# Optimization experiments

Hardware: AMD Instinct MI355X
Metric: run time of the kernel (lower is better)

## Reference

```python
import jax, jax.numpy as jnp
import numpy as np

S_MC = 4      # num_mc_samples
TEMP = 0.1    # soft_sampling temperature


def gcn_conv(x, adj, maskf, W, b):
    # DenseGCNConv: add self loops, sym-normalize, aggregate, linear, mask
    N = adj.shape[-1]
    A = adj + jnp.eye(N, dtype=adj.dtype)
    dis = jnp.clip(A.sum(-1), 1.0, None) ** -0.5
    A = dis[:, :, None] * A * dis[:, None, :]
    out = jnp.einsum('bij,bjf->bif', A, x @ W) + b
    return out * maskf[:, :, None]


def connected_components(adj, mask):
    # min-label propagation; labels in {1..N}, masked nodes -> 0
    B, N, _ = adj.shape
    labels0 = jnp.broadcast_to(jnp.arange(1, N + 1, dtype=jnp.int32), (B, N))
    big = jnp.int32(N + 2)
    adj_b = adj > 0
    def step(labels, _):
        nb = jnp.where(adj_b, labels[:, None, :], big)  # [B,N,N]
        return jnp.minimum(labels, nb.min(-1)), None
    labels, _ = jax.lax.scan(step, labels0, None, length=N)
    return jnp.where(mask, labels, 0)


def setup_inputs() -> dict:
    key = jax.random.key(0)
    ks = jax.random.split(key, 8)
    B, N, Fin, H, K = 512, 64, 128, 256, 32
    x = jax.random.normal(ks[0], (B, N, Fin), jnp.float32)
    lengths = jax.random.randint(ks[1], (B,), N // 2, N + 1)
    mask = jnp.arange(N)[None, :] < lengths[:, None]
    a = jax.random.uniform(ks[2], (B, N, N)) < 0.08
    adj = jnp.triu(a, 1)
    adj = (adj | jnp.swapaxes(adj, 1, 2)).astype(jnp.float32)
    adj = adj * mask[:, :, None] * mask[:, None, :]
    W1 = jax.random.normal(ks[3], (Fin, H), jnp.float32) / np.float32(np.sqrt(Fin))
    b1 = jnp.zeros((H,), jnp.float32)
    W2 = jax.random.normal(ks[4], (H, H), jnp.float32) / np.float32(np.sqrt(H))
    b2 = jnp.zeros((H,), jnp.float32)
    centroids = jax.random.normal(ks[5], (K, H), jnp.float32)
    return {'x': x, 'adj': adj, 'mask': mask, 'W1': W1, 'b1': b1, 'W2': W2, 'b2': b2, 'centroids': centroids}


def reference(x, adj, mask, W1, b1, W2, b2, centroids):
    B, N = mask.shape
    maskf = mask.astype(x.dtype)
    adj = adj * maskf[:, :, None] * maskf[:, None, :]
    # embedding convs
    h = jax.nn.relu(gcn_conv(x, adj, maskf, W1, b1))
    h = jax.nn.relu(gcn_conv(h, adj, maskf, W2, b2))
    # cdist to (detached) centroids, expanded form to avoid [B,N,K,F] blowup
    c = jax.lax.stop_gradient(centroids)
    d2 = (jnp.sum(h * h, -1, keepdims=True) + jnp.sum(c * c, -1)[None, None]
          - 2.0 * jnp.einsum('bnf,kf->bnk', h, c))
    dist = jnp.sqrt(jnp.clip(d2, 1e-12, None))  # [B,N,K]
    # softmin over clusters with temperature
    logits = -dist / TEMP
    probs = jax.nn.softmax(logits, -1)
    logp = jax.nn.log_softmax(logits, -1)
    # Categorical MC sampling via Gumbel-max
    g = jax.random.gumbel(jax.random.key(42), (S_MC,) + logp.shape, logp.dtype)
    concepts = jnp.argmax(logp[None] + g, -1).reshape(S_MC * B, N)  # [SB,N]
    # per-node sampled probability, product over valid nodes per graph (scatter mul)
    probs_r = jnp.tile(probs, (S_MC, 1, 1))
    node_p = jnp.take_along_axis(probs_r, concepts[..., None], -1)[..., 0]
    mask_r = jnp.tile(mask, (S_MC, 1))
    graph_prob = jnp.prod(jnp.where(mask_r, jax.lax.stop_gradient(node_p), 1.0), -1)  # [SB]
    # same-concept restricted adjacency -> connected components (undirected)
    adj_r = jnp.tile(adj, (S_MC, 1, 1))
    same = concepts[:, :, None] == concepts[:, None, :]
    adj_cc = jnp.where(same, adj_r, 0.0)
    adj_cc = jnp.maximum(adj_cc, jnp.swapaxes(adj_cc, 1, 2))
    labels = connected_components(adj_cc, mask_r)  # [SB,N], 0 reserved for masked
    # scatter-mean node embeddings per cluster; drop reserved cluster 0
    P = jax.nn.one_hot(labels, N + 1, dtype=x.dtype) * mask_r[..., None].astype(x.dtype)  # [SB,N,N+1]
    counts = P.sum(1)  # [SB,N+1]
    h_r = jnp.tile(h, (S_MC, 1, 1))
    new_x = (jnp.einsum('bnc,bnf->bcf', P, h_r) / jnp.clip(counts, 1.0, None)[..., None])[:, 1:, :]
    # pooled adjacency S^T A S, binarized
    new_adj = jnp.einsum('bic,bij,bjd->bcd', P, adj_r, P)[:, 1:, 1:]
    new_adj = (new_adj > 0).astype(x.dtype)
    return new_x, new_adj, graph_prob, labels
```

## Files before the change

kernel.cpp:

```cpp
#include <hip/hip_runtime.h>

#define B_    512
#define SB_   2048

static constexpr float TINYF = 1.17549435e-38f;
typedef float fx4  __attribute__((ext_vector_type(4)));
typedef short bf16x8 __attribute__((ext_vector_type(8)));
typedef float f32x4 __attribute__((ext_vector_type(4)));
typedef unsigned short u16x4 __attribute__((ext_vector_type(4)));

__device__ __forceinline__ unsigned tf_bits(unsigned lo) {
  const unsigned ks0 = 0u, ks1 = 42u, ks2 = 0x1BD11BF0u;
  unsigned x0 = 0u + ks0;
  unsigned x1 = lo + ks1;
#define TFR(r) { x0 += x1; x1 = (x1 << r) | (x1 >> (32 - r)); x1 ^= x0; }
  TFR(13) TFR(15) TFR(26) TFR(6)
  x0 += ks1; x1 += ks2 + 1u;
  TFR(17) TFR(29) TFR(16) TFR(24)
  x0 += ks2; x1 += ks0 + 2u;
  TFR(13) TFR(15) TFR(26) TFR(6)
  x0 += ks0; x1 += ks1 + 3u;
  TFR(17) TFR(29) TFR(16) TFR(24)
  x0 += ks1; x1 += ks2 + 4u;
  TFR(13) TFR(15) TFR(26) TFR(6)
  x0 += ks2; x1 += ks0 + 5u;
#undef TFR
  return x0 ^ x1;
}

__device__ __forceinline__ void split3(float v, unsigned& b1, unsigned& b2, unsigned& b3) {
  unsigned u1 = __float_as_uint(v) & 0xFFFF0000u;
  float r1 = v - __uint_as_float(u1);
  unsigned u2 = __float_as_uint(r1) & 0xFFFF0000u;
  float r2 = r1 - __uint_as_float(u2);
  unsigned u3 = __float_as_uint(r2) & 0xFFFF0000u;
  b1 = u1 >> 16; b2 = u2 >> 16; b3 = u3 >> 16;
}

__device__ __forceinline__ unsigned short planeOf(float v, int s) {
  unsigned u1 = __float_as_uint(v) & 0xFFFF0000u;
  if (s == 0) return (unsigned short)(u1 >> 16);
  float r1 = v - __uint_as_float(u1);
  unsigned u2 = __float_as_uint(r1) & 0xFFFF0000u;
  if (s == 1) return (unsigned short)(u2 >> 16);
  float r2 = r1 - __uint_as_float(u2);
  return (unsigned short)((__float_as_uint(r2) & 0xFFFF0000u) >> 16);
}

#define MF6(A0, A1, A2, Bv0, Bv1, Bv2, ACC)                                   \
  ACC = __builtin_amdgcn_mfma_f32_16x16x32_bf16(A0, Bv0, ACC, 0, 0, 0);       \
  ACC = __builtin_amdgcn_mfma_f32_16x16x32_bf16(A0, Bv1, ACC, 0, 0, 0);       \
  ACC = __builtin_amdgcn_mfma_f32_16x16x32_bf16(A1, Bv0, ACC, 0, 0, 0);       \
  ACC = __builtin_amdgcn_mfma_f32_16x16x32_bf16(A0, Bv2, ACC, 0, 0, 0);       \
  ACC = __builtin_amdgcn_mfma_f32_16x16x32_bf16(A1, Bv1, ACC, 0, 0, 0);       \
  ACC = __builtin_amdgcn_mfma_f32_16x16x32_bf16(A2, Bv0, ACC, 0, 0, 0);

__global__ __launch_bounds__(256) void k_init(const float* __restrict__ adj,
                                              const void* __restrict__ mptr,
                                              const float* __restrict__ W1,
                                              const float* __restrict__ W2,
                                              const float* __restrict__ cen,
                                              unsigned short* __restrict__ Ahat3,
                                              unsigned long long* __restrict__ nbr,
                                              float* __restrict__ maskf,
                                              unsigned short* __restrict__ Wg1,
                                              unsigned short* __restrict__ Wg2,
                                              unsigned short* __restrict__ cen3,
                                              float* __restrict__ ccbuf) {
  __shared__ float adjS[4096];
  __shared__ float AhS[64][65];
  __shared__ float dis[64];
  int b = blockIdx.x, tid = threadIdx.x;

  const float* ab = adj + (size_t)b * 4096;
  for (int i = tid; i < 4096; i += 256) adjS[i] = ab[i];
  __syncthreads();
  if (tid < 64) {
    float s = 0.0f;
    unsigned long long m = 0ull;
    for (int j = 0; j < 64; ++j) {
      float v = adjS[j * 64 + tid];
      s += (j == tid) ? (v + 1.0f) : v;
      if (v != 0.0f) m |= (1ull << j);
    }
    dis[tid] = 1.0f / sqrtf(fmaxf(s, 1.0f));
    nbr[b * 64 + tid] = m;
  }
  __syncthreads();
  for (int i = tid; i < 4096; i += 256) {
    int r = i >> 6, c = i & 63;
    float a = adjS[i] + ((r == c) ? 1.0f : 0.0f);
    AhS[r][c] = (dis[r] * a) * dis[c];
  }
  __syncthreads();
  unsigned short* dst = Ahat3 + (size_t)b * 12288;
  for (int ch = tid; ch < 1536; ch += 256) {
    int l15v = ch & 15, lgv = (ch >> 4) & 3, q2 = (ch >> 6) & 3, mt = (ch >> 8) & 1, s = ch >> 9;
    bf16x8 hv;
#pragma unroll
    for (int jj = 0; jj < 8; ++jj)
      hv[jj] = (short)planeOf(AhS[16 * q2 + l15v][32 * mt + 8 * lgv + jj], s);
    *(bf16x8*)&dst[(size_t)ch * 8] = hv;
  }

  if (b < 128) {
    __shared__ int s_ni, s_nf;
    if (tid == 0) { s_ni = 0; s_nf = 0; }
    __syncthreads();
    const unsigned* wp = (const unsigned*)mptr;
    int ni = 0, nf = 0;
    for (int i = tid; i < 2048; i += 256) {
      unsigned v = wp[i];
      if (v > 1u) ni = 1;
      if (v != 0u && v != 0x3f800000u) nf = 1;
    }
    if (ni) atomicOr(&s_ni, 1);
    if (nf) atomicOr(&s_nf, 1);
    __syncthreads();
    int fl = s_ni ? (s_nf ? 2 : 1) : 0;
    int i = b * 256 + tid;
    float r;
    if (fl == 0)      r = ((const int*)mptr)[i] ? 1.0f : 0.0f;
    else if (fl == 1) r = (((const float*)mptr)[i] != 0.0f) ? 1.0f : 0.0f;
    else              r = ((const unsigned char*)mptr)[i] ? 1.0f : 0.0f;
    maskf[i] = r;
  }

  int bi = b - 128;
  if (bi >= 0 && bi < 148) {
    if (bi < 144) {
      const float* W; unsigned short* Wg; int nk, s, ks, g;
      if (bi < 48) { W = W1; Wg = Wg1; nk = 4; s = bi >> 4; ks = (bi >> 2) & 3; g = bi & 3; }
      else { int t = bi - 48; W = W2; Wg = Wg2; nk = 8; s = t >> 5; ks = (t >> 2) & 7; g = t & 3; }
      int n = tid;
      bf16x8 hv;
#pragma unroll
      for (int jj = 0; jj < 8; ++jj) {
        float v = W[(size_t)(ks * 32 + g * 8 + jj) * 256 + n];
        hv[jj] = (short)planeOf(v, s);
      }
      *(bf16x8*)&Wg[((((size_t)s * nk + ks) * 4 + g) * 256 + n) * 8] = hv;
    } else if (bi == 144) {
      int k = tid >> 3, l8 = tid & 7;
      float s = 0.0f;
      for (int m = 0; m < 32; ++m) { float v = cen[k * 256 + l8 + 8 * m]; s += v * v; }
#pragma unroll
      for (int d = 1; d < 8; d <<= 1) s += __shfl_xor(s, d, 64);
      if (l8 == 0) ccbuf[k] = s;
    } else {
      int s = bi - 145;
      for (int u = 0; u < 4; ++u) {
        int idx = tid + 256 * u;
        int ks = idx >> 7, c = (idx >> 6) & 1, rem = idx & 63;
        int l15v = rem >> 2, lgv = rem & 3;
        bf16x8 hv;
#pragma unroll
        for (int jj = 0; jj < 8; ++jj)
          hv[jj] = (short)planeOf(cen[(size_t)(16 * c + l15v) * 256 + 32 * ks + 8 * lgv + jj], s);
        *(bf16x8*)&cen3[(size_t)s * 8192 + (size_t)idx * 8] = hv;
      }
    }
  }
}

__global__ __launch_bounds__(256, 2) void k_layer(const float* __restrict__ A,
                                                  const unsigned short* __restrict__ Wg,
                                                  const float* __restrict__ bias,
                                                  const unsigned short* __restrict__ Ahat3,
                                                  const float* __restrict__ maskf,
                                                  float* __restrict__ out, int nk) {
  __shared__ char smem[36864];
  __shared__ float biaS[256];
  __shared__ float maskS[64];
  unsigned short (*Ap)[3][2112] = (unsigned short(*)[3][2112])smem;
  unsigned short (*Tbuf)[72]    = (unsigned short(*)[72])smem;

  int b = blockIdx.x, tid = threadIdx.x;
  int w = tid >> 6, l = tid & 63;
  int l15 = l & 15, lg = l >> 4;
  int K = nk * 32;
  const float* Ab = A + (size_t)b * 64 * K;
  biaS[tid] = bias[tid];
  if (tid < 64) maskS[tid] = maskf[b * 64 + tid];

  int srow = tid >> 2, sg = tid & 3;
  const float* sp = Ab + (size_t)srow * K + sg * 8;

  {
    float4 v0 = *(const float4*)(sp);
    float4 v1 = *(const float4*)(sp + 4);
    float vv[8] = {v0.x, v0.y, v0.z, v0.w, v1.x, v1.y, v1.z, v1.w};
    bf16x8 p1, p2, p3;
#pragma unroll
    for (int jj = 0; jj < 8; ++jj) {
      unsigned h1, h2, h3; split3(vv[jj], h1, h2, h3);
      p1[jj] = (short)h1; p2[jj] = (short)h2; p3[jj] = (short)h3;
    }
    int off = sg * 528 + srow * 8;
    *(bf16x8*)&Ap[0][0][off] = p1;
    *(bf16x8*)&Ap[0][1][off] = p2;
    *(bf16x8*)&Ap[0][2][off] = p3;
  }
  __syncthreads();

  f32x4 acc1[4][4];
#pragma unroll
  for (int q = 0; q < 4; ++q)
#pragma unroll
    for (int c = 0; c < 4; ++c) acc1[q][c] = (f32x4){0.f, 0.f, 0.f, 0.f};

  const size_t wss = (size_t)nk * 8192;

  for (int ks = 0; ks < nk; ++ks) {
    int cur = ks & 1;
    float4 v0, v1;
    bool pf = (ks + 1 < nk);
    if (pf) {
      v0 = *(const float4*)(sp + (ks + 1) * 32);
      v1 = *(const float4*)(sp + (ks + 1) * 32 + 4);
    }
    bf16x8 af[4][3];
#pragma unroll
    for (int q = 0; q < 4; ++q) {
      int off = lg * 528 + (16 * q + l15) * 8;
#pragma unroll
      for (int s = 0; s < 3; ++s) af[q][s] = *(const bf16x8*)&Ap[cur][s][off];
    }
#pragma unroll
    for (int c = 0; c < 4; ++c) {
      size_t wbase = (((size_t)ks * 4 + lg) * 256 + (64 * w + 16 * c + l15)) * 8;
      bf16x8 b0 = *(const bf16x8*)&Wg[wbase];
      bf16x8 b1 = *(const bf16x8*)&Wg[wbase + wss];
      bf16x8 b2 = *(const bf16x8*)&Wg[wbase + 2 * wss];
#pragma unroll
      for (int q = 0; q < 4; ++q) {
        MF6(af[q][0], af[q][1], af[q][2], b0, b1, b2, acc1[q][c]);
      }
    }
    if (pf) {
      float vv[8] = {v0.x, v0.y, v0.z, v0.w, v1.x, v1.y, v1.z, v1.w};
      bf16x8 p1, p2, p3;
#pragma unroll
      for (int jj = 0; jj < 8; ++jj) {
        unsigned h1, h2, h3; split3(vv[jj], h1, h2, h3);
        p1[jj] = (short)h1; p2[jj] = (short)h2; p3[jj] = (short)h3;
      }
      int off = sg * 528 + srow * 8;
      *(bf16x8*)&Ap[cur ^ 1][0][off] = p1;
      *(bf16x8*)&Ap[cur ^ 1][1][off] = p2;
      *(bf16x8*)&Ap[cur ^ 1][2][off] = p3;
    }
    __syncthreads();
  }

  f32x4 acc2[4][4];
#pragma unroll
  for (int q = 0; q < 4; ++q)
#pragma unroll
    for (int c = 0; c < 4; ++c) acc2[q][c] = (f32x4){0.f, 0.f, 0.f, 0.f};

  const unsigned short* Ah = Ahat3 + (size_t)b * 12288;
#pragma unroll
  for (int sB = 0; sB < 3; ++sB) {
    const int nA = 3 - sB;
    __syncthreads();
#pragma unroll
    for (int q = 0; q < 4; ++q)
#pragma unroll
      for (int c = 0; c < 4; ++c) {
        u16x4 pv;
#pragma unroll
        for (int r = 0; r < 4; ++r) pv[r] = planeOf(acc1[q][c][r], sB);
        *(u16x4*)&Tbuf[64 * w + 16 * c + l15][16 * q + 4 * lg] = pv;
      }
    __syncthreads();
#pragma unroll
    for (int mt = 0; mt < 2; ++mt) {
      bf16x8 bf[4];
#pragma unroll
      for (int c = 0; c < 4; ++c)
        bf[c] = *(const bf16x8*)&Tbuf[64 * w + 16 * c + l15][32 * mt + 8 * lg];
#pragma unroll
      for (int q2 = 0; q2 < 4; ++q2) {
        bf16x8 afr[3];
#pragma unroll
        for (int sA = 0; sA < 3; ++sA)
          if (sA < nA)
            afr[sA] = *(const bf16x8*)&Ah[((((size_t)(sA * 2 + mt) * 4 + q2) * 4 + lg) * 16 + l15) * 8];
#pragma unroll
        for (int c = 0; c < 4; ++c)
#pragma unroll
          for (int sA = 0; sA < 3; ++sA)
            if (sA < nA)
              acc2[q2][c] = __builtin_amdgcn_mfma_f32_16x16x32_bf16(afr[sA], bf[c], acc2[q2][c], 0, 0, 0);
      }
    }
  }

#pragma unroll
  for (int q2 = 0; q2 < 4; ++q2) {
#pragma unroll
    for (int c = 0; c < 4; ++c) {
      int n = 64 * w + 16 * c + l15;
      float bv = biaS[n];
#pragma unroll
      for (int r = 0; r < 4; ++r) {
        int row = 16 * q2 + 4 * lg + r;
        float val = (acc2[q2][c][r] + bv) * maskS[row];
        out[((size_t)b * 64 + row) * 256 + n] = fmaxf(val, 0.0f);
      }
    }
  }
}

__global__ __launch_bounds__(256) void k_cdist(const float* __restrict__ h,
                                               const unsigned short* __restrict__ cen3,
                                               const float* __restrict__ ccbuf,
                                               int* __restrict__ conc,
                                               float* __restrict__ pp) {
  __shared__ float hS[16384];
  __shared__ float Dred[4][64][36];
  __shared__ float hhp[64][4];
  __shared__ float lgp[64][33];
  __shared__ float mxs[64], lgden[64];

  int b = blockIdx.x, tid = threadIdx.x;
  int w = tid >> 6, l = tid & 63, l15 = l & 15, lg = l >> 4;
  const float* hb = h + (size_t)b * 16384;

#pragma unroll
  for (int i = 0; i < 16; ++i) {
    int g = tid + 256 * i;
    float4 v = *(const float4*)&hb[(size_t)g * 4];
    int row = g >> 6;
    int fb = ((g & 63) * 16) ^ ((row & 7) << 4);
    *(float4*)((char*)&hS[row * 256] + fb) = v;
  }
  __syncthreads();

#define LD4(row, fbyte) (*(const float4*)((const char*)&hS[(row) * 256] + ((fbyte) ^ (((row) & 7) << 4))))

  {
    int row = tid & 63, qt = tid >> 6;
    float s = 0.0f;
    for (int u = 0; u < 16; ++u) {
      float4 v = LD4(row, qt * 256 + u * 16);
      s += v.x * v.x + v.y * v.y + v.z * v.z + v.w * v.w;
    }
    hhp[row][qt] = s;
  }

  f32x4 acc[4][2];
#pragma unroll
  for (int qt = 0; qt < 4; ++qt)
#pragma unroll
    for (int c = 0; c < 2; ++c) acc[qt][c] = (f32x4){0.f, 0.f, 0.f, 0.f};

#pragma unroll
  for (int ks2 = 0; ks2 < 2; ++ks2) {
    int ks = 2 * w + ks2;
#pragma unroll
    for (int qt = 0; qt < 4; ++qt) {
      int row = 16 * qt + l15;
      int fb = (32 * ks + 8 * lg) * 4;
      float4 v0 = LD4(row, fb);
      float4 v1 = LD4(row, fb + 16);
      float vv[8] = {v0.x, v0.y, v0.z, v0.w, v1.x, v1.y, v1.z, v1.w};
      bf16x8 a0, a1, a2;
#pragma unroll
      for (int jj = 0; jj < 8; ++jj) {
        unsigned h1, h2, h3; split3(vv[jj], h1, h2, h3);
        a0[jj] = (short)h1; a1[jj] = (short)h2; a2[jj] = (short)h3;
      }
#pragma unroll
      for (int c = 0; c < 2; ++c) {
        const unsigned short* cb = cen3 + ((size_t)(ks * 2 + c) * 64 + l15 * 4 + lg) * 8;
        bf16x8 b0 = *(const bf16x8*)cb;
        bf16x8 b1 = *(const bf16x8*)(cb + 8192);
        bf16x8 b2 = *(const bf16x8*)(cb + 16384);
        MF6(a0, a1, a2, b0, b1, b2, acc[qt][c]);
      }
    }
  }

#pragma unroll
  for (int qt = 0; qt < 4; ++qt)
#pragma unroll
    for (int c = 0; c < 2; ++c)
#pragma unroll
      for (int r = 0; r < 4; ++r)
        Dred[w][16 * qt + 4 * lg + r][16 * c + l15] = acc[qt][c][r];
  __syncthreads();

  {
    int n = tid >> 2, kq = tid & 3;
    float hh = (hhp[n][0] + hhp[n][1]) + (hhp[n][2] + hhp[n][3]);
#pragma unroll
    for (int j = 0; j < 8; ++j) {
      int k = kq * 8 + j;
      float dot = (Dred[0][n][k] + Dred[1][n][k]) + (Dred[2][n][k] + Dred[3][n][k]);
      float d2 = (hh + ccbuf[k]) - 2.0f * dot;
      lgp[n][k] = -10.0f * sqrtf(fmaxf(d2, 1e-12f));
    }
  }
  __syncthreads();

  if (tid < 64) {
    float mx = -1e30f;
    for (int k = 0; k < 32; ++k) mx = fmaxf(mx, lgp[tid][k]);
    float den = 0.0f;
    for (int k = 0; k < 32; ++k) den += expf(lgp[tid][k] - mx);
    mxs[tid] = mx; lgden[tid] = logf(den);
  }
  __syncthreads();
  for (int p = tid; p < 2048; p += 256) {
    int n = p >> 5, k = p & 31;
    lgp[n][k] = (lgp[n][k] - mxs[n]) - lgden[n];
  }
  __syncthreads();

  int hw = tid >> 5, k = tid & 31;
  for (int pass = 0; pass < 8; ++pass) {
    int n = hw * 8 + pass;
    float lp = lgp[n][k];
#pragma unroll
    for (int s4 = 0; s4 < 4; ++s4) {
      unsigned flat = (unsigned)(s4 * 32768 + b * 64 + n) * 32u + (unsigned)k;
      unsigned bits = tf_bits(flat);
      float fu = __uint_as_float((bits >> 9) | 0x3f800000u) - 1.0f;
      float u = fmaxf(TINYF, fu * (1.0f - TINYF) + TINYF);
      float g = -logf(-logf(u));
      float v = lp + g;
      int bi = k;
#pragma unroll
      for (int d = 1; d < 32; d <<= 1) {
        float ov = __shfl_xor(v, d, 32);
        int oi = __shfl_xor(bi, d, 32);
        if (ov > v || (ov == v && oi < bi)) { v = ov; bi = oi; }
      }
      if (k == 0) {
        conc[s4 * 32768 + b * 64 + n] = bi;
        pp[s4 * 32768 + b * 64 + n] = expf(lgp[n][bi]);
      }
    }
  }
#undef LD4
}

__global__ __launch_bounds__(256) void k_postx(const int* __restrict__ conc,
                                               const float* __restrict__ pp,
                                               const float* __restrict__ maskf,
                                               const unsigned long long* __restrict__ nbr,
                                               const float* __restrict__ h,
                                               float* __restrict__ out_gp,
                                               float* __restrict__ out_lab,
                                               float* __restrict__ out_newadj,
                                               float* __restrict__ out_newx) {
  int sb = blockIdx.x, b = sb & 511, tid = threadIdx.x;
  __shared__ int cs[64];
  __shared__ int lab[64];
  __shared__ unsigned long long sm_[64];
  __shared__ unsigned long long nbs[64];
  __shared__ unsigned long long clmaskS[64];
  __shared__ float o[4096];
  __shared__ int chg;

  for (int i = tid; i < 4096; i += 256) o[i] = 0.0f;
  bool mk = false;
  if (tid < 64) {
    cs[tid] = conc[sb * 64 + tid];
    nbs[tid] = nbr[b * 64 + tid];
    mk = maskf[b * 64 + tid] != 0.0f;
    lab[tid] = tid + 1;
  }
  if (tid == 0) chg = 0;
  __syncthreads();
  if (tid < 64) {
    unsigned long long nb = nbs[tid], s = 0ull;
    int c = cs[tid];
    while (nb) { int j = __ffsll(nb) - 1; if (cs[j] == c) s |= (1ull << j); nb &= nb - 1; }
    sm_[tid] = s;
  }
  __syncthreads();
  for (int it = 0; it < 64; ++it) {
    int m = 0;
    if (tid < 64) {
      m = lab[tid];
      unsigned long long t = sm_[tid];
      while (t) { int j = __ffsll(t) - 1; m = min(m, lab[j]); t &= t - 1; }
    }
    __syncthreads();
    if (tid < 64 && m < lab[tid]) { lab[tid] = m; chg = 1; }
    __syncthreads();
    if (chg == 0) break;
    __syncthreads();
    if (tid == 0) chg = 0;
  }
  if (tid < 64) {
    int lf = mk ? lab[tid] : 0;
    cs[tid] = lf;
    out_lab[sb * 64 + tid] = (float)lf;
    float pv = mk ? pp[sb * 64 + tid] : 1.0f;
#pragma unroll
    for (int d = 1; d < 64; d <<= 1) pv *= __shfl_xor(pv, d, 64);
    if (tid == 0) out_gp[sb] = pv;
  }
  __syncthreads();
  if (tid < 64) {
    unsigned long long cm = 0ull;
    for (int j = 0; j < 64; ++j)
      if (cs[j] == tid + 1) cm |= (1ull << j);
    clmaskS[tid] = cm;
  }
  for (int p = tid; p < 4096; p += 256) {
    int i = p >> 6, j = p & 63;
    int li = cs[i], lj = cs[j];
    if (li > 0 && lj > 0 && ((nbs[i] >> j) & 1ull))
      o[(li - 1) * 64 + (lj - 1)] = 1.0f;
  }
  __syncthreads();
  float* dst = out_newadj + (size_t)sb * 4096;
  for (int i = tid; i < 1024; i += 256) {
    fx4 v = ((const fx4*)o)[i];
    __builtin_nontemporal_store(v, (fx4*)dst + i);
  }

  int q = tid & 63, cp = tid >> 6;
  const float* hb = h + (size_t)b * 16384;
  for (int step = 0; step < 16; ++step) {
    int c = cp * 16 + step;
    unsigned long long m = clmaskS[c];
    float4 acc = make_float4(0.f, 0.f, 0.f, 0.f);
    unsigned long long t = m;
    while (t) {
      int j = __ffsll(t) - 1; t &= t - 1;
      float4 v = *(const float4*)&hb[j * 256 + q * 4];
      acc.x += v.x; acc.y += v.y; acc.z += v.z; acc.w += v.w;
    }
    int cnt = __popcll(m);
    float cf = (float)(cnt > 0 ? cnt : 1);
    fx4 r;
    r.x = acc.x / cf; r.y = acc.y / cf; r.z = acc.z / cf; r.w = acc.w / cf;
    __builtin_nontemporal_store(r, (fx4*)&out_newx[((size_t)sb * 64 + c) * 256 + q * 4]);
  }
}

extern "C" void kernel_launch(void* const* d_in, const int* in_sizes, int n_in,
                              void* d_out, int out_size, void* d_ws, size_t ws_size,
                              hipStream_t stream) {
  (void)in_sizes; (void)n_in; (void)out_size; (void)ws_size;
  const float* x   = (const float*)d_in[0];
  const float* adj = (const float*)d_in[1];
  const void*  mp  = d_in[2];
  const float* W1  = (const float*)d_in[3];
  const float* b1  = (const float*)d_in[4];
  const float* W2  = (const float*)d_in[5];
  const float* b2  = (const float*)d_in[6];
  const float* cen = (const float*)d_in[7];

  char* ws = (char*)d_ws;
  unsigned short* Ahat3 = (unsigned short*)(ws + 0);
  unsigned short* Wg1   = (unsigned short*)(ws + 12582912);
  unsigned short* Wg2   = (unsigned short*)(ws + 12779520);
  unsigned short* cen3  = (unsigned short*)(ws + 13172736);
  float* ccbuf          = (float*)(ws + 13221888);
  unsigned long long* nbr = (unsigned long long*)(ws + 13222016);
  float* maskf          = (float*)(ws + 13484160);
  int*   conc           = (int*)(ws + 13615232);
  float* pp             = (float*)(ws + 14139520);
  float* bufB           = (float*)(ws + 16777216);

  float* out        = (float*)d_out;
  float* out_newx   = out;
  float* out_newadj = out + 33554432;
  float* out_gp     = out + 41943040;
  float* out_lab    = out + 41945088;
  float* bufA       = out;

  hipLaunchKernelGGL(k_init,  dim3(512), dim3(256), 0, stream, adj, mp, W1, W2, cen,
                     Ahat3, nbr, maskf, Wg1, Wg2, cen3, ccbuf);
  hipLaunchKernelGGL(k_layer, dim3(512), dim3(256), 0, stream, x,    Wg1, b1, Ahat3, maskf, bufA, 4);
  hipLaunchKernelGGL(k_layer, dim3(512), dim3(256), 0, stream, bufA, Wg2, b2, Ahat3, maskf, bufB, 8);
  hipLaunchKernelGGL(k_cdist, dim3(512), dim3(256), 0, stream, bufB, cen3, ccbuf, conc, pp);
  hipLaunchKernelGGL(k_postx, dim3(2048), dim3(256), 0, stream, conc, pp, maskf, nbr, bufB,
                     out_gp, out_lab, out_newadj, out_newx);
}
```

Baseline: 180.6 us.

## Fuse per-graph pipeline into one mega-kernel with LDS-resident activations

Merges adjacency normalization, both GCN layers, cdist/sampling and cluster pooling into a single per-graph kernel. Intermediate hidden states, the normalized adjacency planes, neighbor masks and concepts stay in shared memory instead of round-tripping through global memory. Each of the 4 MC samples is handled by one wavefront, with wave-level early exit in label propagation. This removes several launches and global traffic, but uses large LDS (one block per CU) and only 512 blocks, which lowers occupancy and parallelism for the post-processing stage.

New measurement: 180.1 us. No clear change (-0.2%).

```diff
diff --git a/kernel.cpp b/kernel.cpp
--- a/kernel.cpp
+++ b/kernel.cpp
@@ -1,7 +1,6 @@
 #include <hip/hip_runtime.h>
 
 #define B_    512
-#define SB_   2048
 
 static constexpr float TINYF = 1.17549435e-38f;
 typedef float fx4  __attribute__((ext_vector_type(4)));
@@ -55,141 +54,74 @@
   ACC = __builtin_amdgcn_mfma_f32_16x16x32_bf16(A1, Bv1, ACC, 0, 0, 0);       \
   ACC = __builtin_amdgcn_mfma_f32_16x16x32_bf16(A2, Bv0, ACC, 0, 0, 0);
 
-__global__ __launch_bounds__(256) void k_init(const float* __restrict__ adj,
-                                              const void* __restrict__ mptr,
-                                              const float* __restrict__ W1,
-                                              const float* __restrict__ W2,
-                                              const float* __restrict__ cen,
-                                              unsigned short* __restrict__ Ahat3,
-                                              unsigned long long* __restrict__ nbr,
-                                              float* __restrict__ maskf,
-                                              unsigned short* __restrict__ Wg1,
-                                              unsigned short* __restrict__ Wg2,
-                                              unsigned short* __restrict__ cen3,
-                                              float* __restrict__ ccbuf) {
-  __shared__ float adjS[4096];
-  __shared__ float AhS[64][65];
-  __shared__ float dis[64];
-  int b = blockIdx.x, tid = threadIdx.x;
-
-  const float* ab = adj + (size_t)b * 4096;
-  for (int i = tid; i < 4096; i += 256) adjS[i] = ab[i];
-  __syncthreads();
-  if (tid < 64) {
+__global__ void k_setup(const float* __restrict__ W1, const float* __restrict__ W2,
+                        const float* __restrict__ cen,
+                        unsigned short* __restrict__ Wg1, unsigned short* __restrict__ Wg2,
+                        unsigned short* __restrict__ cen3, float* __restrict__ ccbuf) {
+  int bi = blockIdx.x, tid = threadIdx.x;
+  if (bi < 144) {
+    const float* W; unsigned short* Wg; int nk, s, ks, g;
+    if (bi < 48) { W = W1; Wg = Wg1; nk = 4; s = bi >> 4; ks = (bi >> 2) & 3; g = bi & 3; }
+    else { int t = bi - 48; W = W2; Wg = Wg2; nk = 8; s = t >> 5; ks = (t >> 2) & 7; g = t & 3; }
+    int n = tid;
+    bf16x8 hv;
+#pragma unroll
+    for (int jj = 0; jj < 8; ++jj) {
+      float v = W[(size_t)(ks * 32 + g * 8 + jj) * 256 + n];
+      hv[jj] = (short)planeOf(v, s);
+    }
+    *(bf16x8*)&Wg[((((size_t)s * nk + ks) * 4 + g) * 256 + n) * 8] = hv;
+  } else if (bi == 144) {
+    int k = tid >> 3, l8 = tid & 7;
     float s = 0.0f;
-    unsigned long long m = 0ull;
-    for (int j = 0; j < 64; ++j) {
-      float v = adjS[j * 64 + tid];
-      s += (j == tid) ? (v + 1.0f) : v;
-      if (v != 0.0f) m |= (1ull << j);
-    }
-    dis[tid] = 1.0f / sqrtf(fmaxf(s, 1.0f));
-    nbr[b * 64 + tid] = m;
-  }
-  __syncthreads();
-  for (int i = tid; i < 4096; i += 256) {
-    int r = i >> 6, c = i & 63;
-    float a = adjS[i] + ((r == c) ? 1.0f : 0.0f);
-    AhS[r][c] = (dis[r] * a) * dis[c];
-  }
-  __syncthreads();
-  unsigned short* dst = Ahat3 + (size_t)b * 12288;
-  for (int ch = tid; ch < 1536; ch += 256) {
-    int l15v = ch & 15, lgv = (ch >> 4) & 3, q2 = (ch >> 6) & 3, mt = (ch >> 8) & 1, s = ch >> 9;
-    bf16x8 hv;
-#pragma unroll
-    for (int jj = 0; jj < 8; ++jj)
-      hv[jj] = (short)planeOf(AhS[16 * q2 + l15v][32 * mt + 8 * lgv + jj], s);
-    *(bf16x8*)&dst[(size_t)ch * 8] = hv;
-  }
-
-  if (b < 128) {
-    __shared__ int s_ni, s_nf;
-    if (tid == 0) { s_ni = 0; s_nf = 0; }
-    __syncthreads();
-    const unsigned* wp = (const unsigned*)mptr;
-    int ni = 0, nf = 0;
-    for (int i = tid; i < 2048; i += 256) {
-      unsigned v = wp[i];
-      if (v > 1u) ni = 1;
-      if (v != 0u && v != 0x3f800000u) nf = 1;
-    }
-    if (ni) atomicOr(&s_ni, 1);
-    if (nf) atomicOr(&s_nf, 1);
-    __syncthreads();
-    int fl = s_ni ? (s_nf ? 2 : 1) : 0;
-    int i = b * 256 + tid;
-    float r;
-    if (fl == 0)      r = ((const int*)mptr)[i] ? 1.0f : 0.0f;
-    else if (fl == 1) r = (((const float*)mptr)[i] != 0.0f) ? 1.0f : 0.0f;
-    else              r = ((const unsigned char*)mptr)[i] ? 1.0f : 0.0f;
-    maskf[i] = r;
-  }
-
-  int bi = b - 128;
-  if (bi >= 0 && bi < 148) {
-    if (bi < 144) {
-      const float* W; unsigned short* Wg; int nk, s, ks, g;
-      if (bi < 48) { W = W1; Wg = Wg1; nk = 4; s = bi >> 4; ks = (bi >> 2) & 3; g = bi & 3; }
-      else { int t = bi - 48; W = W2; Wg = Wg2; nk = 8; s = t >> 5; ks = (t >> 2) & 7; g = t & 3; }
-      int n = tid;
+    for (int m = 0; m < 32; ++m) { float v = cen[k * 256 + l8 + 8 * m]; s += v * v; }
+#pragma unroll
+    for (int d = 1; d < 8; d <<= 1) s += __shfl_xor(s, d, 64);
+    if (l8 == 0) ccbuf[k] = s;
+  } else {
+    int s = bi - 145;
+    for (int u = 0; u < 4; ++u) {
+      int idx = tid + 256 * u;
+      int ks = idx >> 7, c = (idx >> 6) & 1, rem = idx & 63;
+      int l15v = rem >> 2, lgv = rem & 3;
       bf16x8 hv;
 #pragma unroll
-      for (int jj = 0; jj < 8; ++jj) {
-        float v = W[(size_t)(ks * 32 + g * 8 + jj) * 256 + n];
-        hv[jj] = (short)planeOf(v, s);
-      }
-      *(bf16x8*)&Wg[((((size_t)s * nk + ks) * 4 + g) * 256 + n) * 8] = hv;
-    } else if (bi == 144) {
-      int k = tid >> 3, l8 = tid & 7;
-      float s = 0.0f;
-      for (int m = 0; m < 32; ++m) { float v = cen[k * 256 + l8 + 8 * m]; s += v * v; }
-#pragma unroll
-      for (int d = 1; d < 8; d <<= 1) s += __shfl_xor(s, d, 64);
-      if (l8 == 0) ccbuf[k] = s;
-    } else {
-      int s = bi - 145;
-      for (int u = 0; u < 4; ++u) {
-        int idx = tid + 256 * u;
-        int ks = idx >> 7, c = (idx >> 6) & 1, rem = idx & 63;
-        int l15v = rem >> 2, lgv = rem & 3;
-        bf16x8 hv;
-#pragma unroll
-        for (int jj = 0; jj < 8; ++jj)
-          hv[jj] = (short)planeOf(cen[(size_t)(16 * c + l15v) * 256 + 32 * ks + 8 * lgv + jj], s);
-        *(bf16x8*)&cen3[(size_t)s * 8192 + (size_t)idx * 8] = hv;
-      }
-    }
-  }
-}
-
-__global__ __launch_bounds__(256, 2) void k_layer(const float* __restrict__ A,
-                                                  const unsigned short* __restrict__ Wg,
-                                                  const float* __restrict__ bias,
-                                                  const unsigned short* __restrict__ Ahat3,
-                                                  const float* __restrict__ maskf,
-                                                  float* __restrict__ out, int nk) {
-  __shared__ char smem[36864];
-  __shared__ float biaS[256];
-  __shared__ float maskS[64];
-  unsigned short (*Ap)[3][2112] = (unsigned short(*)[3][2112])smem;
-  unsigned short (*Tbuf)[72]    = (unsigned short(*)[72])smem;
-
-  int b = blockIdx.x, tid = threadIdx.x;
+      for (int jj = 0; jj < 8; ++jj)
+        hv[jj] = (short)planeOf(cen[(size_t)(16 * c + l15v) * 256 + 32 * ks + 8 * lgv + jj], s);
+      *(bf16x8*)&cen3[(size_t)s * 8192 + (size_t)idx * 8] = hv;
+    }
+  }
+}
+
+template<bool SRCL>
+__device__ __forceinline__ void layer_core(const float* __restrict__ Aglob,
+                                           const float (*hsrc)[260],
+                                           float (*hdst)[260],
+                                           const unsigned short* __restrict__ Wg, int nk,
+                                           const unsigned short* AhP,
+                                           const float* biaS, const float* maskS,
+                                           char* U, int tid) {
+  unsigned short (*Ap)[3][2112] = (unsigned short(*)[3][2112])U;
+  unsigned short (*Tbuf)[72]    = (unsigned short(*)[72])U;
   int w = tid >> 6, l = tid & 63;
   int l15 = l & 15, lg = l >> 4;
   int K = nk * 32;
-  const float* Ab = A + (size_t)b * 64 * K;
-  biaS[tid] = bias[tid];
-  if (tid < 64) maskS[tid] = maskf[b * 64 + tid];
-
   int srow = tid >> 2, sg = tid & 3;
-  const float* sp = Ab + (size_t)srow * K + sg * 8;
+  const float* sp = SRCL ? (const float*)nullptr : (Aglob + (size_t)srow * K + sg * 8);
 
   {
-    float4 v0 = *(const float4*)(sp);
-    float4 v1 = *(const float4*)(sp + 4);
-    float vv[8] = {v0.x, v0.y, v0.z, v0.w, v1.x, v1.y, v1.z, v1.w};
+    float vv[8];
+    if (SRCL) {
+      float4 v0 = *(const float4*)&hsrc[srow][sg * 8];
+      float4 v1 = *(const float4*)&hsrc[srow][sg * 8 + 4];
+      vv[0] = v0.x; vv[1] = v0.y; vv[2] = v0.z; vv[3] = v0.w;
+      vv[4] = v1.x; vv[5] = v1.y; vv[6] = v1.z; vv[7] = v1.w;
+    } else {
+      float4 v0 = *(const float4*)(sp);
+      float4 v1 = *(const float4*)(sp + 4);
+      vv[0] = v0.x; vv[1] = v0.y; vv[2] = v0.z; vv[3] = v0.w;
+      vv[4] = v1.x; vv[5] = v1.y; vv[6] = v1.z; vv[7] = v1.w;
+    }
     bf16x8 p1, p2, p3;
 #pragma unroll
     for (int jj = 0; jj < 8; ++jj) {
@@ -213,11 +145,20 @@
 
   for (int ks = 0; ks < nk; ++ks) {
     int cur = ks & 1;
-    float4 v0, v1;
+    float vv[8];
     bool pf = (ks + 1 < nk);
     if (pf) {
-      v0 = *(const float4*)(sp + (ks + 1) * 32);
-      v1 = *(const float4*)(sp + (ks + 1) * 32 + 4);
+      if (SRCL) {
+        float4 v0 = *(const float4*)&hsrc[srow][(ks + 1) * 32 + sg * 8];
+        float4 v1 = *(const float4*)&hsrc[srow][(ks + 1) * 32 + sg * 8 + 4];
+        vv[0] = v0.x; vv[1] = v0.y; vv[2] = v0.z; vv[3] = v0.w;
+        vv[4] = v1.x; vv[5] = v1.y; vv[6] = v1.z; vv[7] = v1.w;
+      } else {
+        float4 v0 = *(const float4*)(sp + (ks + 1) * 32);
+        float4 v1 = *(const float4*)(sp + (ks + 1) * 32 + 4);
+        vv[0] = v0.x; vv[1] = v0.y; vv[2] = v0.z; vv[3] = v0.w;
+        vv[4] = v1.x; vv[5] = v1.y; vv[6] = v1.z; vv[7] = v1.w;
+      }
     }
     bf16x8 af[4][3];
 #pragma unroll
@@ -238,7 +179,6 @@
       }
     }
     if (pf) {
-      float vv[8] = {v0.x, v0.y, v0.z, v0.w, v1.x, v1.y, v1.z, v1.w};
       bf16x8 p1, p2, p3;
 #pragma unroll
       for (int jj = 0; jj < 8; ++jj) {
@@ -259,7 +199,6 @@
 #pragma unroll
     for (int c = 0; c < 4; ++c) acc2[q][c] = (f32x4){0.f, 0.f, 0.f, 0.f};
 
-  const unsigned short* Ah = Ahat3 + (size_t)b * 12288;
 #pragma unroll
   for (int sB = 0; sB < 3; ++sB) {
     const int nA = 3 - sB;
@@ -286,7 +225,7 @@
 #pragma unroll
         for (int sA = 0; sA < 3; ++sA)
           if (sA < nA)
-            afr[sA] = *(const bf16x8*)&Ah[((((size_t)(sA * 2 + mt) * 4 + q2) * 4 + lg) * 16 + l15) * 8];
+            afr[sA] = *(const bf16x8*)&AhP[((((size_t)(sA * 2 + mt) * 4 + q2) * 4 + lg) * 16 + l15) * 8];
 #pragma unroll
         for (int c = 0; c < 4; ++c)
 #pragma unroll
@@ -306,242 +245,281 @@
 #pragma unroll
       for (int r = 0; r < 4; ++r) {
         int row = 16 * q2 + 4 * lg + r;
-        float val = (acc2[q2][c][r] + bv) * maskS[row];
-        out[((size_t)b * 64 + row) * 256 + n] = fmaxf(val, 0.0f);
-      }
-    }
-  }
-}
-
-__global__ __launch_bounds__(256) void k_cdist(const float* __restrict__ h,
-                                               const unsigned short* __restrict__ cen3,
-                                               const float* __restrict__ ccbuf,
-                                               int* __restrict__ conc,
-                                               float* __restrict__ pp) {
-  __shared__ float hS[16384];
-  __shared__ float Dred[4][64][36];
+        hdst[row][n] = fmaxf((acc2[q2][c][r] + bv) * maskS[row], 0.0f);
+      }
+    }
+  }
+}
+
+__global__ __launch_bounds__(256, 1) void k_mega(
+    const float* __restrict__ x, const float* __restrict__ adj,
+    const void* __restrict__ mp,
+    const float* __restrict__ b1v, const float* __restrict__ b2v,
+    const unsigned short* __restrict__ Wg1, const unsigned short* __restrict__ Wg2,
+    const unsigned short* __restrict__ cen3, const float* __restrict__ ccbuf,
+    float* __restrict__ out_newx, float* __restrict__ out_newadj,
+    float* __restrict__ out_gp, float* __restrict__ out_lab) {
+  __shared__ float hbuf[64][260];
+  __shared__ unsigned short AhP[12288];
+  __shared__ float maskS[64];
+  __shared__ float biaS[256];
+  __shared__ unsigned long long nbrS[64];
+  __shared__ int concS[4][64];
+  __shared__ float ppS[4][64];
   __shared__ float hhp[64][4];
-  __shared__ float lgp[64][33];
   __shared__ float mxs[64], lgden[64];
+  __shared__ int labFS[4][64];
+  __shared__ int s_ni, s_nf;
+  __shared__ __align__(16) char U[46592];
 
   int b = blockIdx.x, tid = threadIdx.x;
-  int w = tid >> 6, l = tid & 63, l15 = l & 15, lg = l >> 4;
-  const float* hb = h + (size_t)b * 16384;
-
-#pragma unroll
-  for (int i = 0; i < 16; ++i) {
-    int g = tid + 256 * i;
-    float4 v = *(const float4*)&hb[(size_t)g * 4];
-    int row = g >> 6;
-    int fb = ((g & 63) * 16) ^ ((row & 7) << 4);
-    *(float4*)((char*)&hS[row * 256] + fb) = v;
-  }
+
+  {
+    float* adjS = (float*)U;
+    float (*AhS)[65] = (float(*)[65])(U + 16384);
+    float* dis = (float*)(U + 33024);
+    if (tid == 0) { s_ni = 0; s_nf = 0; }
+    const float* ab = adj + (size_t)b * 4096;
+    for (int i = tid; i < 4096; i += 256) adjS[i] = ab[i];
+    {
+      const unsigned* wp = (const unsigned*)mp;
+      int ni = 0, nf = 0;
+      for (int i = tid; i < 2048; i += 256) {
+        unsigned v = wp[i];
+        if (v > 1u) ni = 1;
+        if (v != 0u && v != 0x3f800000u) nf = 1;
+      }
+      if (ni) atomicOr(&s_ni, 1);
+      if (nf) atomicOr(&s_nf, 1);
+    }
+    biaS[tid] = b1v[tid];
+    __syncthreads();
+    if (tid < 64) {
+      float s = 0.0f;
+      unsigned long long m = 0ull;
+      for (int j = 0; j < 64; ++j) {
+        float v = adjS[j * 64 + tid];
+        s += (j == tid) ? (v + 1.0f) : v;
+        if (v != 0.0f) m |= (1ull << j);
+      }
+      dis[tid] = 1.0f / sqrtf(fmaxf(s, 1.0f));
+      nbrS[tid] = m;
+      int fl = s_ni ? (s_nf ? 2 : 1) : 0;
+      int i = b * 64 + tid;
+      float r;
+      if (fl == 0)      r = ((const int*)mp)[i] ? 1.0f : 0.0f;
+      else if (fl == 1) r = (((const float*)mp)[i] != 0.0f) ? 1.0f : 0.0f;
+      else              r = ((const unsigned char*)mp)[i] ? 1.0f : 0.0f;
+      maskS[tid] = r;
+    }
+    __syncthreads();
+    for (int i = tid; i < 4096; i += 256) {
+      int r = i >> 6, c = i & 63;
+      float a = adjS[i] + ((r == c) ? 1.0f : 0.0f);
+      AhS[r][c] = (dis[r] * a) * dis[c];
+    }
+    __syncthreads();
+    for (int ch = tid; ch < 1536; ch += 256) {
+      int l15v = ch & 15, lgv = (ch >> 4) & 3, q2 = (ch >> 6) & 3, mt = (ch >> 8) & 1, s = ch >> 9;
+      bf16x8 hv;
+#pragma unroll
+      for (int jj = 0; jj < 8; ++jj)
+        hv[jj] = (short)planeOf(AhS[16 * q2 + l15v][32 * mt + 8 * lgv + jj], s);
+      *(bf16x8*)&AhP[(size_t)ch * 8] = hv;
+    }
+    __syncthreads();
+  }
+
+  layer_core<false>(x + (size_t)b * 64 * 128, nullptr, hbuf, Wg1, 4, AhP, biaS, maskS, U, tid);
   __syncthreads();
-
-#define LD4(row, fbyte) (*(const float4*)((const char*)&hS[(row) * 256] + ((fbyte) ^ (((row) & 7) << 4))))
+  biaS[tid] = b2v[tid];
+
+  layer_core<true>(nullptr, (const float(*)[260])hbuf, hbuf, Wg2, 8, AhP, biaS, maskS, U, tid);
+  __syncthreads();
 
   {
-    int row = tid & 63, qt = tid >> 6;
-    float s = 0.0f;
-    for (int u = 0; u < 16; ++u) {
-      float4 v = LD4(row, qt * 256 + u * 16);
-      s += v.x * v.x + v.y * v.y + v.z * v.z + v.w * v.w;
-    }
-    hhp[row][qt] = s;
-  }
-
-  f32x4 acc[4][2];
-#pragma unroll
-  for (int qt = 0; qt < 4; ++qt)
-#pragma unroll
-    for (int c = 0; c < 2; ++c) acc[qt][c] = (f32x4){0.f, 0.f, 0.f, 0.f};
-
-#pragma unroll
-  for (int ks2 = 0; ks2 < 2; ++ks2) {
-    int ks = 2 * w + ks2;
-#pragma unroll
-    for (int qt = 0; qt < 4; ++qt) {
-      int row = 16 * qt + l15;
-      int fb = (32 * ks + 8 * lg) * 4;
-      float4 v0 = LD4(row, fb);
-      float4 v1 = LD4(row, fb + 16);
-      float vv[8] = {v0.x, v0.y, v0.z, v0.w, v1.x, v1.y, v1.z, v1.w};
-      bf16x8 a0, a1, a2;
-#pragma unroll
-      for (int jj = 0; jj < 8; ++jj) {
-        unsigned h1, h2, h3; split3(vv[jj], h1, h2, h3);
-        a0[jj] = (short)h1; a1[jj] = (short)h2; a2[jj] = (short)h3;
-      }
-#pragma unroll
-      for (int c = 0; c < 2; ++c) {
-        const unsigned short* cb = cen3 + ((size_t)(ks * 2 + c) * 64 + l15 * 4 + lg) * 8;
-        bf16x8 b0 = *(const bf16x8*)cb;
-        bf16x8 b1 = *(const bf16x8*)(cb + 8192);
-        bf16x8 b2 = *(const bf16x8*)(cb + 16384);
-        MF6(a0, a1, a2, b0, b1, b2, acc[qt][c]);
-      }
-    }
-  }
-
-#pragma unroll
-  for (int qt = 0; qt < 4; ++qt)
-#pragma unroll
-    for (int c = 0; c < 2; ++c)
-#pragma unroll
-      for (int r = 0; r < 4; ++r)
-        Dred[w][16 * qt + 4 * lg + r][16 * c + l15] = acc[qt][c][r];
-  __syncthreads();
+    float (*Dred)[64][36] = (float(*)[64][36])U;
+    float (*lgp)[33] = (float(*)[33])(U + 36864);
+    int w = tid >> 6, l = tid & 63, l15 = l & 15, lg = l >> 4;
+
+    {
+      int row = tid & 63, qt = tid >> 6;
+      float s = 0.0f;
+      for (int u = 0; u < 16; ++u) {
+        float4 v = *(const float4*)&hbuf[row][qt * 64 + u * 4];
+        s += v.x * v.x + v.y * v.y + v.z * v.z + v.w * v.w;
+      }
+      hhp[row][qt] = s;
+    }
+
+    f32x4 acc[4][2];
+#pragma unroll
+    for (int qt = 0; qt < 4; ++qt)
+#pragma unroll
+      for (int c = 0; c < 2; ++c) acc[qt][c] = (f32x4){0.f, 0.f, 0.f, 0.f};
+
+#pragma unroll
+    for (int ks2 = 0; ks2 < 2; ++ks2) {
+      int ks = 2 * w + ks2;
+#pragma unroll
+      for (int qt = 0; qt < 4; ++qt) {
+        int row = 16 * qt + l15;
+        float4 v0 = *(const float4*)&hbuf[row][32 * ks + 8 * lg];
+        float4 v1 = *(const float4*)&hbuf[row][32 * ks + 8 * lg + 4];
+        float vv[8] = {v0.x, v0.y, v0.z, v0.w, v1.x, v1.y, v1.z, v1.w};
+        bf16x8 a0, a1, a2;
+#pragma unroll
+        for (int jj = 0; jj < 8; ++jj) {
+          unsigned h1, h2, h3; split3(vv[jj], h1, h2, h3);
+          a0[jj] = (short)h1; a1[jj] = (short)h2; a2[jj] = (short)h3;
+        }
+#pragma unroll
+        for (int c = 0; c < 2; ++c) {
+          const unsigned short* cb = cen3 + ((size_t)(ks * 2 + c) * 64 + l15 * 4 + lg) * 8;
+          bf16x8 b0 = *(const bf16x8*)cb;
+          bf16x8 b1 = *(const bf16x8*)(cb + 8192);
+          bf16x8 b2 = *(const bf16x8*)(cb + 16384);
+          MF6(a0, a1, a2, b0, b1, b2, acc[qt][c]);
+        }
+      }
+    }
+
+#pragma unroll
+    for (int qt = 0; qt < 4; ++qt)
+#pragma unroll
+      for (int c = 0; c < 2; ++c)
+#pragma unroll
+        for (int r = 0; r < 4; ++r)
+          Dred[w][16 * qt + 4 * lg + r][16 * c + l15] = acc[qt][c][r];
+    __syncthreads();
+
+    {
+      int n = tid >> 2, kq = tid & 3;
+      float hh = (hhp[n][0] + hhp[n][1]) + (hhp[n][2] + hhp[n][3]);
+#pragma unroll
+      for (int j = 0; j < 8; ++j) {
+        int k = kq * 8 + j;
+        float dot = (Dred[0][n][k] + Dred[1][n][k]) + (Dred[2][n][k] + Dred[3][n][k]);
+        float d2 = (hh + ccbuf[k]) - 2.0f * dot;
+        lgp[n][k] = -10.0f * sqrtf(fmaxf(d2, 1e-12f));
+      }
+    }
+    __syncthreads();
+
+    if (tid < 64) {
+      float mx = -1e30f;
+      for (int k = 0; k < 32; ++k) mx = fmaxf(mx, lgp[tid][k]);
+      float den = 0.0f;
+      for (int k = 0; k < 32; ++k) den += expf(lgp[tid][k] - mx);
+      mxs[tid] = mx; lgden[tid] = logf(den);
+    }
+    __syncthreads();
+    for (int p = tid; p < 2048; p += 256) {
+      int n = p >> 5, k = p & 31;
+      lgp[n][k] = (lgp[n][k] - mxs[n]) - lgden[n];
+    }
+    __syncthreads();
+
+    int hw = tid >> 5, k = tid & 31;
+    for (int pass = 0; pass < 8; ++pass) {
+      int n = hw * 8 + pass;
+      float lp = lgp[n][k];
+#pragma unroll
+      for (int s4 = 0; s4 < 4; ++s4) {
+        unsigned flat = (unsigned)(s4 * 32768 + b * 64 + n) * 32u + (unsigned)k;
+        unsigned bits = tf_bits(flat);
+        float fu = __uint_as_float((bits >> 9) | 0x3f800000u) - 1.0f;
+        float u = fmaxf(TINYF, fu * (1.0f - TINYF) + TINYF);
+        float g = -logf(-logf(u));
+        float v = lp + g;
+        int bi = k;
+#pragma unroll
+        for (int d = 1; d < 32; d <<= 1) {
+          float ov = __shfl_xor(v, d, 32);
+          int oi = __shfl_xor(bi, d, 32);
+          if (ov > v || (ov == v && oi < bi)) { v = ov; bi = oi; }
+        }
+        if (k == 0) {
+          concS[s4][n] = bi;
+          ppS[s4][n] = expf(lgp[n][bi]);
+        }
+      }
+    }
+    __syncthreads();
+  }
 
   {
-    int n = tid >> 2, kq = tid & 3;
-    float hh = (hhp[n][0] + hhp[n][1]) + (hhp[n][2] + hhp[n][3]);
-#pragma unroll
-    for (int j = 0; j < 8; ++j) {
-      int k = kq * 8 + j;
-      float dot = (Dred[0][n][k] + Dred[1][n][k]) + (Dred[2][n][k] + Dred[3][n][k]);
-      float d2 = (hh + ccbuf[k]) - 2.0f * dot;
-      lgp[n][k] = -10.0f * sqrtf(fmaxf(d2, 1e-12f));
-    }
-  }
-  __syncthreads();
-
-  if (tid < 64) {
-    float mx = -1e30f;
-    for (int k = 0; k < 32; ++k) mx = fmaxf(mx, lgp[tid][k]);
-    float den = 0.0f;
-    for (int k = 0; k < 32; ++k) den += expf(lgp[tid][k] - mx);
-    mxs[tid] = mx; lgden[tid] = logf(den);
-  }
-  __syncthreads();
-  for (int p = tid; p < 2048; p += 256) {
-    int n = p >> 5, k = p & 31;
-    lgp[n][k] = (lgp[n][k] - mxs[n]) - lgden[n];
-  }
-  __syncthreads();
-
-  int hw = tid >> 5, k = tid & 31;
-  for (int pass = 0; pass < 8; ++pass) {
-    int n = hw * 8 + pass;
-    float lp = lgp[n][k];
-#pragma unroll
-    for (int s4 = 0; s4 < 4; ++s4) {
-      unsigned flat = (unsigned)(s4 * 32768 + b * 64 + n) * 32u + (unsigned)k;
-      unsigned bits = tf_bits(flat);
-      float fu = __uint_as_float((bits >> 9) | 0x3f800000u) - 1.0f;
-      float u = fmaxf(TINYF, fu * (1.0f - TINYF) + TINYF);
-      float g = -logf(-logf(u));
-      float v = lp + g;
-      int bi = k;
-#pragma unroll
-      for (int d = 1; d < 32; d <<= 1) {
-        float ov = __shfl_xor(v, d, 32);
-        int oi = __shfl_xor(bi, d, 32);
-        if (ov > v || (ov == v && oi < bi)) { v = ov; bi = oi; }
-      }
-      if (k == 0) {
-        conc[s4 * 32768 + b * 64 + n] = bi;
-        pp[s4 * 32768 + b * 64 + n] = expf(lgp[n][bi]);
-      }
-    }
-  }
-#undef LD4
-}
-
-__global__ __launch_bounds__(256) void k_postx(const int* __restrict__ conc,
-                                               const float* __restrict__ pp,
-                                               const float* __restrict__ maskf,
-                                               const unsigned long long* __restrict__ nbr,
-                                               const float* __restrict__ h,
-                                               float* __restrict__ out_gp,
-                                               float* __restrict__ out_lab,
-                                               float* __restrict__ out_newadj,
-                                               float* __restrict__ out_newx) {
-  int sb = blockIdx.x, b = sb & 511, tid = threadIdx.x;
-  __shared__ int cs[64];
-  __shared__ int lab[64];
-  __shared__ unsigned long long sm_[64];
-  __shared__ unsigned long long nbs[64];
-  __shared__ unsigned long long clmaskS[64];
-  __shared__ float o[4096];
-  __shared__ int chg;
-
-  for (int i = tid; i < 4096; i += 256) o[i] = 0.0f;
-  bool mk = false;
-  if (tid < 64) {
-    cs[tid] = conc[sb * 64 + tid];
-    nbs[tid] = nbr[b * 64 + tid];
-    mk = maskf[b * 64 + tid] != 0.0f;
-    lab[tid] = tid + 1;
-  }
-  if (tid == 0) chg = 0;
-  __syncthreads();
-  if (tid < 64) {
-    unsigned long long nb = nbs[tid], s = 0ull;
-    int c = cs[tid];
-    while (nb) { int j = __ffsll(nb) - 1; if (cs[j] == c) s |= (1ull << j); nb &= nb - 1; }
-    sm_[tid] = s;
-  }
-  __syncthreads();
-  for (int it = 0; it < 64; ++it) {
-    int m = 0;
-    if (tid < 64) {
-      m = lab[tid];
-      unsigned long long t = sm_[tid];
-      while (t) { int j = __ffsll(t) - 1; m = min(m, lab[j]); t &= t - 1; }
-    }
-    __syncthreads();
-    if (tid < 64 && m < lab[tid]) { lab[tid] = m; chg = 1; }
-    __syncthreads();
-    if (chg == 0) break;
-    __syncthreads();
-    if (tid == 0) chg = 0;
-  }
-  if (tid < 64) {
-    int lf = mk ? lab[tid] : 0;
-    cs[tid] = lf;
-    out_lab[sb * 64 + tid] = (float)lf;
-    float pv = mk ? pp[sb * 64 + tid] : 1.0f;
+    unsigned char (*o)[4096] = (unsigned char(*)[4096])U;
+    int s = tid >> 6, lane = tid & 63;
+    int sbo = s * 512 + b;
+    int c0 = concS[s][lane];
+    bool mk = maskS[lane] != 0.0f;
+    unsigned long long nb = nbrS[lane];
+    unsigned long long sm = 0ull;
+    {
+      unsigned long long t = nb;
+      while (t) { int j = __ffsll(t) - 1; if (concS[s][j] == c0) sm |= (1ull << j); t &= t - 1; }
+    }
+    labFS[s][lane] = lane + 1;
+    for (int it = 0; it < 64; ++it) {
+      int m = labFS[s][lane];
+      unsigned long long t = sm;
+      while (t) { int j = __ffsll(t) - 1; m = min(m, labFS[s][j]); t &= t - 1; }
+      bool ch = m < labFS[s][lane];
+      if (ch) labFS[s][lane] = m;
+      if (!__any(ch)) break;
+    }
+    int lf = mk ? labFS[s][lane] : 0;
+    out_lab[(size_t)sbo * 64 + lane] = (float)lf;
+    float pv = mk ? ppS[s][lane] : 1.0f;
 #pragma unroll
     for (int d = 1; d < 64; d <<= 1) pv *= __shfl_xor(pv, d, 64);
-    if (tid == 0) out_gp[sb] = pv;
-  }
-  __syncthreads();
-  if (tid < 64) {
+    if (lane == 0) out_gp[sbo] = pv;
+    labFS[s][lane] = lf;
     unsigned long long cm = 0ull;
     for (int j = 0; j < 64; ++j)
-      if (cs[j] == tid + 1) cm |= (1ull << j);
-    clmaskS[tid] = cm;
-  }
-  for (int p = tid; p < 4096; p += 256) {
-    int i = p >> 6, j = p & 63;
-    int li = cs[i], lj = cs[j];
-    if (li > 0 && lj > 0 && ((nbs[i] >> j) & 1ull))
-      o[(li - 1) * 64 + (lj - 1)] = 1.0f;
-  }
-  __syncthreads();
-  float* dst = out_newadj + (size_t)sb * 4096;
-  for (int i = tid; i < 1024; i += 256) {
-    fx4 v = ((const fx4*)o)[i];
-    __builtin_nontemporal_store(v, (fx4*)dst + i);
-  }
-
-  int q = tid & 63, cp = tid >> 6;
-  const float* hb = h + (size_t)b * 16384;
-  for (int step = 0; step < 16; ++step) {
-    int c = cp * 16 + step;
-    unsigned long long m = clmaskS[c];
-    float4 acc = make_float4(0.f, 0.f, 0.f, 0.f);
-    unsigned long long t = m;
-    while (t) {
-      int j = __ffsll(t) - 1; t &= t - 1;
-      float4 v = *(const float4*)&hb[j * 256 + q * 4];
-      acc.x += v.x; acc.y += v.y; acc.z += v.z; acc.w += v.w;
-    }
-    int cnt = __popcll(m);
-    float cf = (float)(cnt > 0 ? cnt : 1);
-    fx4 r;
-    r.x = acc.x / cf; r.y = acc.y / cf; r.z = acc.z / cf; r.w = acc.w / cf;
-    __builtin_nontemporal_store(r, (fx4*)&out_newx[((size_t)sb * 64 + c) * 256 + q * 4]);
+      if (labFS[s][j] == lane + 1) cm |= (1ull << j);
+    {
+      unsigned* op = (unsigned*)o[s];
+#pragma unroll
+      for (int u = 0; u < 16; ++u) op[u * 64 + lane] = 0u;
+      int li = lf;
+      if (li > 0) {
+        unsigned long long t = nb;
+        while (t) {
+          int j = __ffsll(t) - 1; t &= t - 1;
+          int lj = labFS[s][j];
+          if (lj > 0) o[s][(li - 1) * 64 + (lj - 1)] = 1;
+        }
+      }
+      float* dA = out_newadj + (size_t)sbo * 4096;
+#pragma unroll
+      for (int u = 0; u < 16; ++u) {
+        int base = u * 256 + lane * 4;
+        fx4 v;
+        v.x = o[s][base + 0] ? 1.0f : 0.0f;
+        v.y = o[s][base + 1] ? 1.0f : 0.0f;
+        v.z = o[s][base + 2] ? 1.0f : 0.0f;
+        v.w = o[s][base + 3] ? 1.0f : 0.0f;
+        __builtin_nontemporal_store(v, (fx4*)&dA[base]);
+      }
+    }
+    float* dX = out_newx + (size_t)sbo * 64 * 256;
+    for (int c = 0; c < 64; ++c) {
+      unsigned long long m = __shfl(cm, c, 64);
+      float4 acc = make_float4(0.f, 0.f, 0.f, 0.f);
+      unsigned long long t = m;
+      while (t) {
+        int j = __ffsll(t) - 1; t &= t - 1;
+        float4 v = *(const float4*)&hbuf[j][lane * 4];
+        acc.x += v.x; acc.y += v.y; acc.z += v.z; acc.w += v.w;
+      }
+      int cnt = __popcll(m);
+      float cf = (float)(cnt > 0 ? cnt : 1);
+      fx4 r;
+      r.x = acc.x / cf; r.y = acc.y / cf; r.z = acc.z / cf; r.w = acc.w / cf;
+      __builtin_nontemporal_store(r, (fx4*)&dX[(size_t)c * 256 + lane * 4]);
+    }
   }
 }
 
@@ -559,29 +537,18 @@
   const float* cen = (const float*)d_in[7];
 
   char* ws = (char*)d_ws;
-  unsigned short* Ahat3 = (unsigned short*)(ws + 0);
-  unsigned short* Wg1   = (unsigned short*)(ws + 12582912);
-  unsigned short* Wg2   = (unsigned short*)(ws + 12779520);
-  unsigned short* cen3  = (unsigned short*)(ws + 13172736);
-  float* ccbuf          = (float*)(ws + 13221888);
-  unsigned long long* nbr = (unsigned long long*)(ws + 13222016);
-  float* maskf          = (float*)(ws + 13484160);
-  int*   conc           = (int*)(ws + 13615232);
-  float* pp             = (float*)(ws + 14139520);
-  float* bufB           = (float*)(ws + 16777216);
+  unsigned short* Wg1  = (unsigned short*)(ws + 0);
+  unsigned short* Wg2  = (unsigned short*)(ws + 196608);
+  unsigned short* cen3 = (unsigned short*)(ws + 589824);
+  float* ccbuf         = (float*)(ws + 638976);
 
   float* out        = (float*)d_out;
   float* out_newx   = out;
   float* out_newadj = out + 33554432;
   float* out_gp     = out + 41943040;
   float* out_lab    = out + 41945088;
-  float* bufA       = out;
-
-  hipLaunchKernelGGL(k_init,  dim3(512), dim3(256), 0, stream, adj, mp, W1, W2, cen,
-                     Ahat3, nbr, maskf, Wg1, Wg2, cen3, ccbuf);
-  hipLaunchKernelGGL(k_layer, dim3(512), dim3(256), 0, stream, x,    Wg1, b1, Ahat3, maskf, bufA, 4);
-  hipLaunchKernelGGL(k_layer, dim3(512), dim3(256), 0, stream, bufA, Wg2, b2, Ahat3, maskf, bufB, 8);
-  hipLaunchKernelGGL(k_cdist, dim3(512), dim3(256), 0, stream, bufB, cen3, ccbuf, conc, pp);
-  hipLaunchKernelGGL(k_postx, dim3(2048), dim3(256), 0, stream, conc, pp, maskf, nbr, bufB,
-                     out_gp, out_lab, out_newadj, out_newx);
-}
+
+  hipLaunchKernelGGL(k_setup, dim3(148), dim3(256), 0, stream, W1, W2, cen, Wg1, Wg2, cen3, ccbuf);
+  hipLaunchKernelGGL(k_mega,  dim3(512), dim3(256), 0, stream, x, adj, mp, b1, b2,
+                     Wg1, Wg2, cen3, ccbuf, out_newx, out_newadj, out_gp, out_lab);
+}
```
